# Kernel optimization log

Hardware: AMD Instinct MI355X
Metric: run time of the kernel (lower is better)

## Reference

```python
import math
import jax, jax.numpy as jnp
import numpy as np

N_EMBD = 1024
N_HEAD = 16
B, T = 2, 2048
MASK_VALUE = -1000000.0


def setup_inputs() -> dict:
    key = jax.random.key(0)
    ks = jax.random.split(key, 10)
    s = 1.0 / math.sqrt(N_EMBD)
    x = jax.random.normal(ks[0], (B, T, N_EMBD), dtype=jnp.float32)
    # torch.nn.Linear weights are (out_features, in_features)
    Wq = jax.random.normal(ks[1], (N_EMBD, N_EMBD), dtype=jnp.float32) * s
    bq = jax.random.normal(ks[2], (N_EMBD,), dtype=jnp.float32) * s
    Wk = jax.random.normal(ks[3], (N_EMBD, N_EMBD), dtype=jnp.float32) * s
    bk = jax.random.normal(ks[4], (N_EMBD,), dtype=jnp.float32) * s
    Wv = jax.random.normal(ks[5], (N_EMBD, N_EMBD), dtype=jnp.float32) * s
    bv = jax.random.normal(ks[6], (N_EMBD,), dtype=jnp.float32) * s
    Wp = jax.random.normal(ks[7], (N_EMBD, N_EMBD), dtype=jnp.float32) * s
    bp = jax.random.normal(ks[8], (N_EMBD,), dtype=jnp.float32) * s
    # causal attn mask (B, T, T): 1 where attention allowed
    attn_mask = jnp.broadcast_to(
        jnp.tril(jnp.ones((T, T), dtype=jnp.int32))[None], (B, T, T))
    valid_input_mask = jnp.ones((B, T), dtype=jnp.int32)
    return {"x": x, "Wq": Wq, "bq": bq, "Wk": Wk, "bk": bk,
            "Wv": Wv, "bv": bv, "Wp": Wp, "bp": bp,
            "attn_mask": attn_mask, "valid_input_mask": valid_input_mask}


def reference(x, Wq, bq, Wk, bk, Wv, bv, Wp, bp, attn_mask, valid_input_mask):
    Bb, Tt, C = x.shape
    H = N_HEAD
    d = C // H
    # projections (torch Linear: x @ W.T + b), split into heads -> (B, H, T, d)
    def heads(y):
        return y.reshape(Bb, Tt, H, d).transpose(0, 2, 1, 3)
    q = heads(x @ Wq.T + bq)
    k = heads(x @ Wk.T + bk)
    v = heads(x @ Wv.T + bv)
    # attention scores (B, H, T, T)
    att = jnp.einsum('bhtd,bhsd->bhts', q, k) * (1.0 / math.sqrt(d))
    att = jnp.where(attn_mask[:, None, :, :] == 0, MASK_VALUE, att)
    att = jnp.where(valid_input_mask[:, None, None, :] == 0, MASK_VALUE, att)
    att = jax.nn.softmax(att, axis=-1)
    y = jnp.einsum('bhts,bhsd->bhtd', att, v)
    y = y.transpose(0, 2, 1, 3).reshape(Bb, Tt, C)
    return y @ Wp.T + bp
```

## Files before the change

kernel.cpp:

```cpp
#include <hip/hip_runtime.h>
#include <hip/hip_bf16.h>
#include <stdint.h>

typedef unsigned short u16;
typedef __attribute__((ext_vector_type(8))) short bf16x8;
typedef __attribute__((ext_vector_type(4))) float f32x4;

#define AS1 __attribute__((address_space(1)))
#define AS3 __attribute__((address_space(3)))

__device__ __forceinline__ void gload_lds16(const void* g, void* l) {
  __builtin_amdgcn_global_load_lds((const AS1 void*)g, (AS3 void*)l, 16, 0, 0);
}

__device__ __forceinline__ u16 f2bf(float f) {
  union { float f; uint32_t u; } v; v.f = f;
  uint32_t r = v.u + 0x7FFFu + ((v.u >> 16) & 1u);
  return (u16)(r >> 16);
}

__global__ void cvt_all(const float* __restrict__ x,
                        const float* __restrict__ w0, const float* __restrict__ w1,
                        const float* __restrict__ w2, const float* __restrict__ w3,
                        u16* __restrict__ x16, u16* __restrict__ w16) {
  int i = blockIdx.x * 256 + threadIdx.x;
  const float* src; u16* dst; int off;
  if (i < 1048576) { src = x; dst = x16; off = i; }
  else {
    int j = i - 1048576; int w = j >> 18; off = j & 262143;
    src = (w == 0) ? w0 : (w == 1) ? w1 : (w == 2) ? w2 : w3;
    dst = w16 + (size_t)w * 1048576;
  }
  float4 v = ((const float4*)src)[off];
  uint64_t pk = (uint64_t)f2bf(v.x) | ((uint64_t)f2bf(v.y) << 16) |
                ((uint64_t)f2bf(v.z) << 32) | ((uint64_t)f2bf(v.w) << 48);
  ((uint64_t*)dst)[off] = pk;
}

#define BM 128
#define BN 128
#define BK 32

template<int MODE>
__global__ __launch_bounds__(256, 2)
void gemm_bt(const u16* __restrict__ A, const u16* __restrict__ Bw,
             const float* __restrict__ bias0, const float* __restrict__ bias1,
             const float* __restrict__ bias2, void* __restrict__ Out,
             int M, int N, int K)
{
  __shared__ __align__(16) u16 As[BM * BK];
  __shared__ __align__(16) u16 Bs[BN * BK];
  const int tid = threadIdx.x;
  const int lane = tid & 63, wid = tid >> 6;
  const int lr = lane & 15, lg = lane >> 4;
  const int m0 = blockIdx.y * BM, n0 = blockIdx.x * BN;
  const int z = blockIdx.z;
  const u16* Bz = Bw + (size_t)z * N * K;
  const float* bias = (MODE == 0) ? (z == 0 ? bias0 : (z == 1 ? bias1 : bias2)) : bias0;
  const int wm = (wid >> 1) * 64, wn = (wid & 1) * 64;

  f32x4 acc[4][4] = {};

  for (int kt = 0; kt < K; kt += BK) {
    __syncthreads();
#pragma unroll
    for (int i = 0; i < 2; ++i) {
      int cb = (i * 4 + wid) * 64;
      int c = cb + lane;
      int row = c >> 2, kc = (c & 3) * 8;
      gload_lds16(A  + (size_t)(m0 + row) * K + kt + kc, (void*)&As[(size_t)cb * 8]);
      gload_lds16(Bz + (size_t)(n0 + row) * K + kt + kc, (void*)&Bs[(size_t)cb * 8]);
    }
    __syncthreads();

    bf16x8 af[4], bfr[4];
#pragma unroll
    for (int mf = 0; mf < 4; ++mf) af[mf]  = *(const bf16x8*)&As[(wm + mf * 16 + lr) * BK + lg * 8];
#pragma unroll
    for (int nf = 0; nf < 4; ++nf) bfr[nf] = *(const bf16x8*)&Bs[(wn + nf * 16 + lr) * BK + lg * 8];
#pragma unroll
    for (int mf = 0; mf < 4; ++mf)
#pragma unroll
      for (int nf = 0; nf < 4; ++nf)
        acc[mf][nf] = __builtin_amdgcn_mfma_f32_16x16x32_bf16(af[mf], bfr[nf], acc[mf][nf], 0, 0, 0);
  }

#pragma unroll
  for (int nf = 0; nf < 4; ++nf) {
    float bv = bias[n0 + wn + nf * 16 + lr];
#pragma unroll
    for (int mf = 0; mf < 4; ++mf)
#pragma unroll
      for (int r = 0; r < 4; ++r) {
        int m = m0 + wm + mf * 16 + lg * 4 + r;
        int n = n0 + wn + nf * 16 + lr;
        float v = acc[mf][nf][r] + bv;
        if (MODE == 0) {
          if (z == 0) v *= 0.125f;
          size_t addr = ((size_t)(m >> 11) * 16 + (n >> 6)) * (size_t)(2048 * 64)
                      + (size_t)(m & 2047) * 64 + (n & 63);
          ((u16*)Out)[(size_t)z * 4194304 + addr] = f2bf(v);
        } else {
          ((float*)Out)[(size_t)m * N + n] = v;
        }
      }
  }
}

__global__ void transpose_v(const u16* __restrict__ v, u16* __restrict__ vt) {
  __shared__ __align__(16) u16 t[64][72];
  const int tid = threadIdx.x;
  const int s0 = blockIdx.x * 64;
  const int bh = blockIdx.y;
  const u16* src = v + (size_t)bh * 2048 * 64;
  u16* dst = vt + (size_t)bh * 64 * 2048;
#pragma unroll
  for (int i = 0; i < 2; ++i) {
    int c = tid + i * 256;
    int r = c >> 3, col = (c & 7) * 8;
    *(bf16x8*)&t[r][col] = *(const bf16x8*)&src[(size_t)(s0 + r) * 64 + col];
  }
  __syncthreads();
#pragma unroll
  for (int i = 0; i < 2; ++i) {
    int c = tid + i * 256;
    int d = c >> 3, sc = (c & 7) * 8;
    bf16x8 o;
#pragma unroll
    for (int j = 0; j < 8; ++j) o[j] = (short)t[sc + j][d];
    *(bf16x8*)&dst[(size_t)d * 2048 + s0 + sc] = o;
  }
}

__global__ __launch_bounds__(512, 4)
void attn_fwd(const u16* __restrict__ q, const u16* __restrict__ k,
              const u16* __restrict__ vt, u16* __restrict__ y)
{
  __shared__ __align__(16) u16 Ks[128 * 64];
  __shared__ __align__(16) u16 Vs[64 * 128];
  __shared__ __align__(16) u16 Ps[8][16 * 136];
  const int tid = threadIdx.x, lane = tid & 63, wid = tid >> 6;
  const int lr = lane & 15, lg = lane >> 4;
  const int bx = blockIdx.x, by = blockIdx.y;
  const int r4 = (bx + by) & 15;
  const int qt = (by & 16) ? r4 : 15 - r4;
  const int q0 = qt * 128;
  const int bh = by;
  const u16* qg = q + (size_t)bh * 2048 * 64;
  const u16* kg = k + (size_t)bh * 2048 * 64;
  const u16* vg = vt + (size_t)bh * 64 * 2048;
  const int trow0 = q0 + wid * 16;
  const int tq = trow0 + lr;

  bf16x8 qa[2];
#pragma unroll
  for (int kk = 0; kk < 2; ++kk)
    qa[kk] = *(const bf16x8*)&qg[(size_t)(trow0 + lr) * 64 + kk * 32 + lg * 8];

  const int l8 = lane >> 3, s8 = lane & 7;
  const int kr0 = wid * 16 + l8;
  const int vd  = wid * 8 + l8;
  const u16* kld = kg + (size_t)kr0 * 64 + s8 * 8;
  const u16* vld = vg + (size_t)vd * 2048 + s8 * 8;
  u16* kst0 = &Ks[kr0 * 64 + (s8 ^ l8) * 8];
  u16* kst1 = &Ks[(kr0 + 8) * 64 + (s8 ^ l8) * 8];
  u16* vst0 = &Vs[vd * 128 + ((s8    ) ^ (vd & 7)) * 8];
  u16* vst1 = &Vs[vd * 128 + ((s8 + 8) ^ (vd & 7)) * 8];

  bf16x8 ldK0, ldK1, ldV0, ldV1;
  ldK0 = *(const bf16x8*)(kld);
  ldK1 = *(const bf16x8*)(kld + 8 * 64);
  ldV0 = *(const bf16x8*)(vld);
  ldV1 = *(const bf16x8*)(vld + 64);

  f32x4 oacc[4] = {};
  float mrun = -1e30f, lrun = 0.f;
  const int nk2 = qt + 1;
  const int xsl = lr & 7;

  for (int j = 0; j < nk2; ++j) {
    *(bf16x8*)kst0 = ldK0;  *(bf16x8*)kst1 = ldK1;
    *(bf16x8*)vst0 = ldV0;  *(bf16x8*)vst1 = ldV1;
    if (j + 1 < nk2) {
      const u16* kn = kld + (size_t)(j + 1) * 8192;
      const u16* vn = vld + (size_t)(j + 1) * 128;
      ldK0 = *(const bf16x8*)(kn);
      ldK1 = *(const bf16x8*)(kn + 8 * 64);
      ldV0 = *(const bf16x8*)(vn);
      ldV1 = *(const bf16x8*)(vn + 64);
    }
    asm volatile("s_waitcnt lgkmcnt(0)" ::: "memory");
    __builtin_amdgcn_s_barrier();

    f32x4 sacc[8] = {};
#pragma unroll
    for (int kk = 0; kk < 2; ++kk) {
#pragma unroll
      for (int h = 0; h < 2; ++h) {
        bf16x8 kb[4];
#pragma unroll
        for (int sf = 0; sf < 4; ++sf)
          kb[sf] = *(const bf16x8*)&Ks[((h * 4 + sf) * 16 + lr) * 64 + (((kk * 4 + lg) ^ xsl) * 8)];
#pragma unroll
        for (int sf = 0; sf < 4; ++sf)
          sacc[h * 4 + sf] = __builtin_amdgcn_mfma_f32_16x16x32_bf16(kb[sf], qa[kk], sacc[h * 4 + sf], 0, 0, 0);
      }
    }

    if (j == qt) {
#pragma unroll
      for (int sf = 0; sf < 8; ++sf)
#pragma unroll
        for (int r = 0; r < 4; ++r) {
          int s = j * 128 + sf * 16 + lg * 4 + r;
          if (s > tq) sacc[sf][r] = -1e30f;
        }
    }

    float m01 = fmaxf(fmaxf(fmaxf(sacc[0][0], sacc[0][1]), fmaxf(sacc[0][2], sacc[0][3])),
                      fmaxf(fmaxf(sacc[1][0], sacc[1][1]), fmaxf(sacc[1][2], sacc[1][3])));
    float m23 = fmaxf(fmaxf(fmaxf(sacc[2][0], sacc[2][1]), fmaxf(sacc[2][2], sacc[2][3])),
                      fmaxf(fmaxf(sacc[3][0], sacc[3][1]), fmaxf(sacc[3][2], sacc[3][3])));
    float m45 = fmaxf(fmaxf(fmaxf(sacc[4][0], sacc[4][1]), fmaxf(sacc[4][2], sacc[4][3])),
                      fmaxf(fmaxf(sacc[5][0], sacc[5][1]), fmaxf(sacc[5][2], sacc[5][3])));
    float m67 = fmaxf(fmaxf(fmaxf(sacc[6][0], sacc[6][1]), fmaxf(sacc[6][2], sacc[6][3])),
                      fmaxf(fmaxf(sacc[7][0], sacc[7][1]), fmaxf(sacc[7][2], sacc[7][3])));
    float mx = fmaxf(fmaxf(m01, m23), fmaxf(m45, m67));
    mx = fmaxf(mx, __shfl_xor(mx, 16));
    mx = fmaxf(mx, __shfl_xor(mx, 32));
    if (!__all(mx - mrun <= 8.0f)) {
      float mn = fmaxf(mrun, mx);
      float scn = __expf(mrun - mn);
      mrun = mn;
      lrun *= scn;
      float scr[4];
#pragma unroll
      for (int r = 0; r < 4; ++r) scr[r] = __shfl(scn, lg * 4 + r);
#pragma unroll
      for (int nf = 0; nf < 4; ++nf)
#pragma unroll
        for (int r = 0; r < 4; ++r) oacc[nf][r] *= scr[r];
    }
    float rs = 0.f;
#pragma unroll
    for (int sf = 0; sf < 8; ++sf)
#pragma unroll
      for (int r = 0; r < 4; ++r) {
        float p = __expf(sacc[sf][r] - mrun);
        sacc[sf][r] = p;
        rs += p;
      }
    rs += __shfl_xor(rs, 16);
    rs += __shfl_xor(rs, 32);
    lrun += rs;

#pragma unroll
    for (int sf = 0; sf < 8; ++sf) {
      union { ushort4 u; uint2 d; } pk_;
      pk_.u.x = f2bf(sacc[sf][0]); pk_.u.y = f2bf(sacc[sf][1]);
      pk_.u.z = f2bf(sacc[sf][2]); pk_.u.w = f2bf(sacc[sf][3]);
      *(uint2*)&Ps[wid][lr * 136 + sf * 16 + lg * 4] = pk_.d;
    }

#pragma unroll
    for (int kk = 0; kk < 4; ++kk) {
      bf16x8 pa = *(const bf16x8*)&Ps[wid][lr * 136 + kk * 32 + lg * 8];
      bf16x8 vb[4];
#pragma unroll
      for (int nf = 0; nf < 4; ++nf)
        vb[nf] = *(const bf16x8*)&Vs[(nf * 16 + lr) * 128 + (((kk * 4 + lg) ^ xsl) * 8)];
#pragma unroll
      for (int nf = 0; nf < 4; ++nf)
        oacc[nf] = __builtin_amdgcn_mfma_f32_16x16x32_bf16(pa, vb[nf], oacc[nf], 0, 0, 0);
    }

    asm volatile("s_waitcnt lgkmcnt(0)" ::: "memory");
    __builtin_amdgcn_s_barrier();
  }

  const int b = bh >> 4, h = bh & 15;
#pragma unroll
  for (int r = 0; r < 4; ++r) {
    float lshf = __shfl(lrun, lg * 4 + r);
    float inv = 1.f / lshf;
    int t = trow0 + lg * 4 + r;
#pragma unroll
    for (int nf = 0; nf < 4; ++nf) {
      int n = nf * 16 + lr;
      y[((size_t)b * 2048 + t) * 1024 + h * 64 + n] = f2bf(oacc[nf][r] * inv);
    }
  }
}

extern "C" void kernel_launch(void* const* d_in, const int* in_sizes, int n_in,
                              void* d_out, int out_size, void* d_ws, size_t ws_size,
                              hipStream_t stream) {
  const float* x  = (const float*)d_in[0];
  const float* Wq = (const float*)d_in[1];
  const float* bq = (const float*)d_in[2];
  const float* Wk = (const float*)d_in[3];
  const float* bk = (const float*)d_in[4];
  const float* Wv = (const float*)d_in[5];
  const float* bv = (const float*)d_in[6];
  const float* Wp = (const float*)d_in[7];
  const float* bp = (const float*)d_in[8];

  char* ws = (char*)d_ws;
  u16* x16  = (u16*)(ws + (size_t)0);
  u16* w16  = (u16*)(ws + ((size_t)8  << 20));
  u16* q16  = (u16*)(ws + ((size_t)16 << 20));
  u16* k16  = (u16*)(ws + ((size_t)24 << 20));
  u16* v16  = (u16*)(ws + ((size_t)32 << 20));
  u16* vt16 = (u16*)(ws + ((size_t)40 << 20));
  u16* y16  = x16;

  cvt_all<<<8192, 256, 0, stream>>>(x, Wq, Wk, Wv, Wp, x16, w16);
  gemm_bt<0><<<dim3(8, 32, 3), 256, 0, stream>>>(x16, w16, bq, bk, bv, (void*)q16, 4096, 1024, 1024);
  transpose_v<<<dim3(32, 32), 256, 0, stream>>>(v16, vt16);
  attn_fwd<<<dim3(16, 32), 512, 0, stream>>>(q16, k16, vt16, y16);
  gemm_bt<1><<<dim3(8, 32, 1), 256, 0, stream>>>(y16, w16 + 3 * 1048576, bp, bp, bp, d_out, 4096, 1024, 1024);
}
```

Baseline: 119.0 us.

## Split attention into 64-row query tiles with 4 waves, use exp2 softmax

The attention kernel moves from 128-row query tiles with 8 waves to 64-row tiles with 4 waves and twice as many blocks. Each wave now loads more of the K/V tile into shared memory. This is meant to balance the causal workload more finely and raise occupancy. Softmax now uses exp2 with log2(e) folded into the Q scale, the rescale threshold is raised, and the scalar bf16 packing is replaced by the packed __float22bfloat162_rn intrinsic. The cost is that each K/V tile is reloaded by twice as many blocks.

After: 143.5 us. 20.5% more time.

```diff
diff --git a/kernel.cpp b/kernel.cpp
--- a/kernel.cpp
+++ b/kernel.cpp
@@ -32,9 +32,10 @@
     dst = w16 + (size_t)w * 1048576;
   }
   float4 v = ((const float4*)src)[off];
-  uint64_t pk = (uint64_t)f2bf(v.x) | ((uint64_t)f2bf(v.y) << 16) |
-                ((uint64_t)f2bf(v.z) << 32) | ((uint64_t)f2bf(v.w) << 48);
-  ((uint64_t*)dst)[off] = pk;
+  union { __hip_bfloat162 h[2]; uint64_t u; } o;
+  o.h[0] = __float22bfloat162_rn(float2{v.x, v.y});
+  o.h[1] = __float22bfloat162_rn(float2{v.z, v.w});
+  ((uint64_t*)dst)[off] = o.u;
 }
 
 #define BM 128
@@ -96,7 +97,7 @@
         int n = n0 + wn + nf * 16 + lr;
         float v = acc[mf][nf][r] + bv;
         if (MODE == 0) {
-          if (z == 0) v *= 0.125f;
+          if (z == 0) v *= 0.18033688f;
           size_t addr = ((size_t)(m >> 11) * 16 + (n >> 6)) * (size_t)(2048 * 64)
                       + (size_t)(m & 2047) * 64 + (n & 63);
           ((u16*)Out)[(size_t)z * 4194304 + addr] = f2bf(v);
@@ -132,25 +133,25 @@
   }
 }
 
-__global__ __launch_bounds__(512, 4)
+__global__ __launch_bounds__(256, 4)
 void attn_fwd(const u16* __restrict__ q, const u16* __restrict__ k,
               const u16* __restrict__ vt, u16* __restrict__ y)
 {
   __shared__ __align__(16) u16 Ks[128 * 64];
   __shared__ __align__(16) u16 Vs[64 * 128];
-  __shared__ __align__(16) u16 Ps[8][16 * 136];
+  __shared__ __align__(16) u16 Ps[4][16 * 136];
   const int tid = threadIdx.x, lane = tid & 63, wid = tid >> 6;
   const int lr = lane & 15, lg = lane >> 4;
-  const int bx = blockIdx.x, by = blockIdx.y;
-  const int r4 = (bx + by) & 15;
-  const int qt = (by & 16) ? r4 : 15 - r4;
-  const int q0 = qt * 128;
-  const int bh = by;
+  const int qt = 31 - ((blockIdx.x + blockIdx.y) & 31);
+  const int q0 = qt * 64;
+  const int bh = blockIdx.y;
   const u16* qg = q + (size_t)bh * 2048 * 64;
   const u16* kg = k + (size_t)bh * 2048 * 64;
   const u16* vg = vt + (size_t)bh * 64 * 2048;
   const int trow0 = q0 + wid * 16;
   const int tq = trow0 + lr;
+  const int dtile = qt >> 1;
+  const int nkt = dtile + 1;
 
   bf16x8 qa[2];
 #pragma unroll
@@ -158,36 +159,47 @@
     qa[kk] = *(const bf16x8*)&qg[(size_t)(trow0 + lr) * 64 + kk * 32 + lg * 8];
 
   const int l8 = lane >> 3, s8 = lane & 7;
-  const int kr0 = wid * 16 + l8;
-  const int vd  = wid * 8 + l8;
-  const u16* kld = kg + (size_t)kr0 * 64 + s8 * 8;
-  const u16* vld = vg + (size_t)vd * 2048 + s8 * 8;
-  u16* kst0 = &Ks[kr0 * 64 + (s8 ^ l8) * 8];
-  u16* kst1 = &Ks[(kr0 + 8) * 64 + (s8 ^ l8) * 8];
-  u16* vst0 = &Vs[vd * 128 + ((s8    ) ^ (vd & 7)) * 8];
-  u16* vst1 = &Vs[vd * 128 + ((s8 + 8) ^ (vd & 7)) * 8];
-
-  bf16x8 ldK0, ldK1, ldV0, ldV1;
-  ldK0 = *(const bf16x8*)(kld);
-  ldK1 = *(const bf16x8*)(kld + 8 * 64);
-  ldV0 = *(const bf16x8*)(vld);
-  ldV1 = *(const bf16x8*)(vld + 64);
+  const u16* kld = kg + (size_t)(wid * 32 + l8) * 64 + s8 * 8;
+  const u16* vld = vg + (size_t)(wid * 16 + l8) * 2048 + s8 * 8;
+  u16* kst[4]; u16* vst[4];
+#pragma unroll
+  for (int m = 0; m < 4; ++m)
+    kst[m] = &Ks[(wid * 32 + l8 + 8 * m) * 64 + ((s8 ^ l8) * 8)];
+#pragma unroll
+  for (int m = 0; m < 2; ++m) {
+    int d = wid * 16 + l8 + 8 * m;
+    vst[2 * m]     = &Vs[d * 128 + ((s8 ^ l8) * 8)];
+    vst[2 * m + 1] = &Vs[d * 128 + (((s8 + 8) ^ l8) * 8)];
+  }
+
+  bf16x8 ldK[4], ldV[4];
+#pragma unroll
+  for (int m = 0; m < 4; ++m) ldK[m] = *(const bf16x8*)(kld + (size_t)(8 * m) * 64);
+#pragma unroll
+  for (int m = 0; m < 2; ++m) {
+    ldV[2 * m]     = *(const bf16x8*)(vld + (size_t)(8 * m) * 2048);
+    ldV[2 * m + 1] = *(const bf16x8*)(vld + (size_t)(8 * m) * 2048 + 64);
+  }
 
   f32x4 oacc[4] = {};
   float mrun = -1e30f, lrun = 0.f;
-  const int nk2 = qt + 1;
   const int xsl = lr & 7;
 
-  for (int j = 0; j < nk2; ++j) {
-    *(bf16x8*)kst0 = ldK0;  *(bf16x8*)kst1 = ldK1;
-    *(bf16x8*)vst0 = ldV0;  *(bf16x8*)vst1 = ldV1;
-    if (j + 1 < nk2) {
+  for (int j = 0; j < nkt; ++j) {
+#pragma unroll
+    for (int m = 0; m < 4; ++m) *(bf16x8*)kst[m] = ldK[m];
+#pragma unroll
+    for (int m = 0; m < 4; ++m) *(bf16x8*)vst[m] = ldV[m];
+    if (j + 1 < nkt) {
       const u16* kn = kld + (size_t)(j + 1) * 8192;
       const u16* vn = vld + (size_t)(j + 1) * 128;
-      ldK0 = *(const bf16x8*)(kn);
-      ldK1 = *(const bf16x8*)(kn + 8 * 64);
-      ldV0 = *(const bf16x8*)(vn);
-      ldV1 = *(const bf16x8*)(vn + 64);
+#pragma unroll
+      for (int m = 0; m < 4; ++m) ldK[m] = *(const bf16x8*)(kn + (size_t)(8 * m) * 64);
+#pragma unroll
+      for (int m = 0; m < 2; ++m) {
+        ldV[2 * m]     = *(const bf16x8*)(vn + (size_t)(8 * m) * 2048);
+        ldV[2 * m + 1] = *(const bf16x8*)(vn + (size_t)(8 * m) * 2048 + 64);
+      }
     }
     asm volatile("s_waitcnt lgkmcnt(0)" ::: "memory");
     __builtin_amdgcn_s_barrier();
@@ -207,7 +219,7 @@
       }
     }
 
-    if (j == qt) {
+    if (j == dtile) {
 #pragma unroll
       for (int sf = 0; sf < 8; ++sf)
 #pragma unroll
@@ -228,9 +240,9 @@
     float mx = fmaxf(fmaxf(m01, m23), fmaxf(m45, m67));
     mx = fmaxf(mx, __shfl_xor(mx, 16));
     mx = fmaxf(mx, __shfl_xor(mx, 32));
-    if (!__all(mx - mrun <= 8.0f)) {
+    if (!__all(mx - mrun <= 11.5f)) {
       float mn = fmaxf(mrun, mx);
-      float scn = __expf(mrun - mn);
+      float scn = exp2f(mrun - mn);
       mrun = mn;
       lrun *= scn;
       float scr[4];
@@ -246,7 +258,7 @@
     for (int sf = 0; sf < 8; ++sf)
 #pragma unroll
       for (int r = 0; r < 4; ++r) {
-        float p = __expf(sacc[sf][r] - mrun);
+        float p = exp2f(sacc[sf][r] - mrun);
         sacc[sf][r] = p;
         rs += p;
       }
@@ -256,9 +268,9 @@
 
 #pragma unroll
     for (int sf = 0; sf < 8; ++sf) {
-      union { ushort4 u; uint2 d; } pk_;
-      pk_.u.x = f2bf(sacc[sf][0]); pk_.u.y = f2bf(sacc[sf][1]);
-      pk_.u.z = f2bf(sacc[sf][2]); pk_.u.w = f2bf(sacc[sf][3]);
+      union { __hip_bfloat162 h[2]; uint2 d; } pk_;
+      pk_.h[0] = __float22bfloat162_rn(float2{sacc[sf][0], sacc[sf][1]});
+      pk_.h[1] = __float22bfloat162_rn(float2{sacc[sf][2], sacc[sf][3]});
       *(uint2*)&Ps[wid][lr * 136 + sf * 16 + lg * 4] = pk_.d;
     }
 
@@ -317,6 +329,6 @@
   cvt_all<<<8192, 256, 0, stream>>>(x, Wq, Wk, Wv, Wp, x16, w16);
   gemm_bt<0><<<dim3(8, 32, 3), 256, 0, stream>>>(x16, w16, bq, bk, bv, (void*)q16, 4096, 1024, 1024);
   transpose_v<<<dim3(32, 32), 256, 0, stream>>>(v16, vt16);
-  attn_fwd<<<dim3(16, 32), 512, 0, stream>>>(q16, k16, vt16, y16);
+  attn_fwd<<<dim3(32, 32), 256, 0, stream>>>(q16, k16, vt16, y16);
   gemm_bt<1><<<dim3(8, 32, 1), 256, 0, stream>>>(y16, w16 + 3 * 1048576, bp, bp, bp, d_out, 4096, 1024, 1024);
 }
```
